# Kernel optimization log

Measured on AMD Instinct MI355X. Metric: run time of the kernel, lower is better.

## Reference

```python
import jax, jax.numpy as jnp
import numpy as np

N_NODES = 50000


def setup_inputs() -> dict:
    key = jax.random.key(0)
    ks = jax.random.split(key, 6)
    F_IN, F_HID, N_EDGES = 128, 512, 800000
    x = jax.random.normal(ks[0], (N_NODES, F_IN), dtype=jnp.float32)
    edge_index = jax.random.randint(ks[1], (2, N_EDGES), 0, N_NODES, dtype=jnp.int64)
    W1 = jax.random.normal(ks[2], (F_IN, F_HID), dtype=jnp.float32) * (1.0 / np.sqrt(F_IN))
    b1 = jnp.zeros((F_HID,), dtype=jnp.float32)
    W2 = jax.random.normal(ks[3], (F_HID, F_IN), dtype=jnp.float32) * (1.0 / np.sqrt(F_HID))
    b2 = jnp.zeros((F_IN,), dtype=jnp.float32)
    eps = jnp.zeros((), dtype=jnp.float32)  # train_eps=True, init 0
    return {"x": x, "edge_index": edge_index, "W1": W1, "b1": b1, "W2": W2, "b2": b2, "eps": eps}


def reference(x, edge_index, W1, b1, W2, b2, eps):
    # GINConv: out = MLP((1+eps)*x + sum_{j in N(i)} x_j)
    src, dst = edge_index[0], edge_index[1]
    agg = jax.ops.segment_sum(x[src], dst, num_segments=N_NODES)  # [N, F]
    h = (1.0 + eps) * x + agg
    h = jax.nn.relu(h @ W1 + b1)
    out = h @ W2 + b2
    return out
```

## Files before the change

kernel.cpp:

```cpp
#include <hip/hip_runtime.h>
#include <hip/hip_bf16.h>

#define N_NODES 50000
#define F_IN    128
#define F_HID   512
#define N_EDGES 800000

#define NBKT 782
#define RCAP 384
#define BINCAP 1280

typedef __bf16 bf16x2 __attribute__((ext_vector_type(2)));
typedef __bf16 bf16x4 __attribute__((ext_vector_type(4)));
typedef __bf16 bf16x8 __attribute__((ext_vector_type(8)));
typedef float  f32x4  __attribute__((ext_vector_type(4)));

#define NB_X 6250
#define NB_W 32
#define NB_CZ 98
__global__ __launch_bounds__(256) void prep(const float* __restrict__ x,
                                            const float* __restrict__ W1,
                                            const float* __restrict__ W2,
                                            __bf16* __restrict__ xb,
                                            __bf16* __restrict__ w1f,
                                            __bf16* __restrict__ w2f,
                                            int* __restrict__ bcnt) {
    int b = blockIdx.x, tid = threadIdx.x;
    if (b < NB_X) {
        int i = b * 256 + tid;
        float4 v = ((const float4*)x)[i];
        bf16x4 o = {(__bf16)v.x, (__bf16)v.y, (__bf16)v.z, (__bf16)v.w};
        ((bf16x4*)xb)[i] = o;
    } else if (b < NB_X + NB_W) {
        int t = (b - NB_X) * 256 + tid;
        int lane = t & 63, kk = (t >> 6) & 3, nt = (t >> 8) & 7, c = (t >> 11) & 3;
        int q = lane >> 4, l16 = lane & 15;
        bf16x8 o;
        #pragma unroll
        for (int j = 0; j < 8; ++j)
            o[j] = (__bf16)W1[(kk * 32 + q * 8 + j) * F_HID + c * 128 + nt * 16 + l16];
        *(bf16x8*)(w1f + (size_t)t * 8) = o;
    } else if (b < NB_X + 2 * NB_W) {
        int t = (b - NB_X - NB_W) * 256 + tid;
        int lane = t & 63, kk = (t >> 6) & 3, nt = (t >> 8) & 7, c = (t >> 11) & 3;
        int q = lane >> 4, l16 = lane & 15;
        bf16x8 o;
        #pragma unroll
        for (int j = 0; j < 8; ++j)
            o[j] = (__bf16)W2[(c * 128 + kk * 32 + q * 8 + j) * F_IN + nt * 16 + l16];
        *(bf16x8*)(w2f + (size_t)t * 8) = o;
    } else {
        int i = (b - NB_X - 2 * NB_W) * 256 + tid;
        if (i < NBKT * 8 * 4) {
            int4 z = {0, 0, 0, 0};
            ((int4*)bcnt)[i] = z;
        }
    }
}

__global__ __launch_bounds__(256) void bucket_fill(const int* __restrict__ ei,
                                                   int* __restrict__ bcnt,
                                                   int* __restrict__ entries) {
    int e = blockIdx.x * 256 + threadIdx.x;
    if (e >= N_EDGES) return;
    int src = ei[e];
    int dst = ei[N_EDGES + e];
    int cell = (dst >> 6) * 8 + (blockIdx.x & 7);
    int p = atomicAdd(&bcnt[cell * 16], 1);
    if (p < RCAP)
        entries[cell * RCAP + p] = ((dst & 63) << 16) | src;
}

__global__ __launch_bounds__(256) void bucket_bin(const int* __restrict__ bcnt,
                                                  const int* __restrict__ entries,
                                                  unsigned short* __restrict__ binned,
                                                  unsigned int* __restrict__ meta) {
    __shared__ int deg[64], base[64], cur[64];
    const int tid = threadIdx.x;
    const int bkt = blockIdx.x;

    if (tid < 64) deg[tid] = 0;
    __syncthreads();

    #pragma unroll
    for (int r = 0; r < 8; ++r) {
        int cnt = bcnt[(bkt * 8 + r) * 16];
        cnt = cnt < RCAP ? cnt : RCAP;
        const int* eb = entries + (size_t)(bkt * 8 + r) * RCAP;
        for (int i = tid; i < cnt; i += 256)
            atomicAdd(&deg[eb[i] >> 16], 1);
    }
    __syncthreads();

    if (tid == 0) {
        int s = 0;
        for (int n = 0; n < 64; ++n) { base[n] = s; s += deg[n]; }
    }
    __syncthreads();

    if (tid < 64) {
        cur[tid] = base[tid];
        int node = bkt * 64 + tid;
        if (node < N_NODES)
            meta[node] = ((unsigned int)deg[tid] << 20) | (unsigned int)(bkt * BINCAP + base[tid]);
    }
    __syncthreads();

    #pragma unroll
    for (int r = 0; r < 8; ++r) {
        int cnt = bcnt[(bkt * 8 + r) * 16];
        cnt = cnt < RCAP ? cnt : RCAP;
        const int* eb = entries + (size_t)(bkt * 8 + r) * RCAP;
        for (int i = tid; i < cnt; i += 256) {
            int en = eb[i];
            int p = atomicAdd(&cur[en >> 16], 1);
            if (p < BINCAP)
                binned[(size_t)bkt * BINCAP + p] = (unsigned short)(en & 0xffff);
        }
    }
}

__global__ __launch_bounds__(256) void gather_agg(const __bf16* __restrict__ xb,
                                                  const unsigned int* __restrict__ meta,
                                                  const unsigned short* __restrict__ binned,
                                                  const float* __restrict__ eps,
                                                  __bf16* __restrict__ agg) {
    int node = blockIdx.x * 4 + (threadIdx.x >> 6);
    int lane = threadIdx.x & 63;
    int q = lane >> 4, l16 = lane & 15;
    if (node >= N_NODES) return;
    const float s = 1.0f + eps[0];

    unsigned int m = meta[node];
    int deg = m >> 20;
    const unsigned short* bin = binned + (m & 0xFFFFF);

    float acc[8];
    #pragma unroll
    for (int i = 0; i < 8; ++i) acc[i] = 0.0f;
    if (q == 0) {
        bf16x8 self = *(const bf16x8*)(xb + (size_t)node * F_IN + l16 * 8);
        #pragma unroll
        for (int i = 0; i < 8; ++i) acc[i] = (float)self[i] * s;
    }

    int j = q;
    for (; j + 4 < deg; j += 8) {
        int s0 = bin[j];
        int s1 = bin[j + 4];
        bf16x8 v0 = *(const bf16x8*)(xb + (size_t)s0 * F_IN + l16 * 8);
        bf16x8 v1 = *(const bf16x8*)(xb + (size_t)s1 * F_IN + l16 * 8);
        #pragma unroll
        for (int i = 0; i < 8; ++i) acc[i] += (float)v0[i] + (float)v1[i];
    }
    if (j < deg) {
        bf16x8 v = *(const bf16x8*)(xb + (size_t)bin[j] * F_IN + l16 * 8);
        #pragma unroll
        for (int i = 0; i < 8; ++i) acc[i] += (float)v[i];
    }

    #pragma unroll
    for (int i = 0; i < 8; ++i) {
        acc[i] += __shfl_xor(acc[i], 16);
        acc[i] += __shfl_xor(acc[i], 32);
    }
    if (q == 0) {
        bf16x8 o;
        #pragma unroll
        for (int i = 0; i < 8; ++i) o[i] = (__bf16)acc[i];
        *(bf16x8*)(agg + (size_t)node * F_IN + l16 * 8) = o;
    }
}

__global__ __launch_bounds__(256) void fused_mlp(const __bf16* __restrict__ A,
                                                 const __bf16* __restrict__ w1f,
                                                 const __bf16* __restrict__ w2f,
                                                 const float* __restrict__ b1,
                                                 const float* __restrict__ b2,
                                                 float* __restrict__ out) {
    __shared__ __attribute__((aligned(16))) __bf16 Hb[4096];

    const int tid  = threadIdx.x;
    const int wave = tid >> 6;
    const int lane = tid & 63;
    const int q = lane >> 4, l16 = lane & 15;
    const int m0 = blockIdx.x * 32;

    bf16x8 a_reg[2][4];
    #pragma unroll
    for (int mi = 0; mi < 2; ++mi) {
        int m = m0 + mi * 16 + l16;
        #pragma unroll
        for (int kk = 0; kk < 4; ++kk) {
            if (m < N_NODES)
                a_reg[mi][kk] = *(const bf16x8*)(A + (size_t)m * F_IN + kk * 32 + q * 8);
            else {
                __bf16 z = (__bf16)0.0f;
                a_reg[mi][kk] = (bf16x8){z, z, z, z, z, z, z, z};
            }
        }
    }

    f32x4 acc_o[2][2];
    #pragma unroll
    for (int ni = 0; ni < 2; ++ni) {
        float bv = b2[wave * 32 + ni * 16 + l16];
        f32x4 b4 = {bv, bv, bv, bv};
        acc_o[0][ni] = b4;
        acc_o[1][ni] = b4;
    }

    for (int c = 0; c < 4; ++c) {
        f32x4 acc_h[2][2];
        #pragma unroll
        for (int ni = 0; ni < 2; ++ni) {
            float bv = b1[c * 128 + wave * 32 + ni * 16 + l16];
            f32x4 b4 = {bv, bv, bv, bv};
            acc_h[0][ni] = b4;
            acc_h[1][ni] = b4;
        }
        #pragma unroll
        for (int kk = 0; kk < 4; ++kk) {
            bf16x8 bw[2];
            #pragma unroll
            for (int ni = 0; ni < 2; ++ni)
                bw[ni] = *(const bf16x8*)(w1f +
                    ((size_t)((c * 8 + wave * 2 + ni) * 4 + kk) << 9) + lane * 8);
            #pragma unroll
            for (int mi = 0; mi < 2; ++mi)
                #pragma unroll
                for (int ni = 0; ni < 2; ++ni)
                    acc_h[mi][ni] = __builtin_amdgcn_mfma_f32_16x16x32_bf16(
                        a_reg[mi][kk], bw[ni], acc_h[mi][ni], 0, 0, 0);
        }
        #pragma unroll
        for (int mi = 0; mi < 2; ++mi)
            #pragma unroll
            for (int ni = 0; ni < 2; ++ni)
                #pragma unroll
                for (int r = 0; r < 4; ++r)
                    Hb[(((mi * 4 + wave) * 64 + (ni * 2 + (l16 >> 3)) * 16 + q * 4 + r) << 3)
                       + (l16 & 7)] = (__bf16)fmaxf(acc_h[mi][ni][r], 0.0f);
        __syncthreads();

        #pragma unroll
        for (int kk = 0; kk < 4; ++kk) {
            bf16x8 am[2], bw[2];
            #pragma unroll
            for (int mi = 0; mi < 2; ++mi)
                am[mi] = *(const bf16x8*)&Hb[((mi * 4 + kk) * 64 + lane) << 3];
            #pragma unroll
            for (int ni = 0; ni < 2; ++ni)
                bw[ni] = *(const bf16x8*)(w2f +
                    ((size_t)((c * 8 + wave * 2 + ni) * 4 + kk) << 9) + lane * 8);
            #pragma unroll
            for (int mi = 0; mi < 2; ++mi)
                #pragma unroll
                for (int ni = 0; ni < 2; ++ni)
                    acc_o[mi][ni] = __builtin_amdgcn_mfma_f32_16x16x32_bf16(
                        am[mi], bw[ni], acc_o[mi][ni], 0, 0, 0);
        }
        __syncthreads();
    }

    #pragma unroll
    for (int mi = 0; mi < 2; ++mi)
        #pragma unroll
        for (int ni = 0; ni < 2; ++ni)
            #pragma unroll
            for (int r = 0; r < 4; ++r) {
                int m = m0 + mi * 16 + q * 4 + r;
                if (m < N_NODES)
                    out[(size_t)m * F_IN + wave * 32 + ni * 16 + l16] = acc_o[mi][ni][r];
            }
}

extern "C" void kernel_launch(void* const* d_in, const int* in_sizes, int n_in,
                              void* d_out, int out_size, void* d_ws, size_t ws_size,
                              hipStream_t stream) {
    const float* x   = (const float*)d_in[0];
    const int*   ei  = (const int*)d_in[1];
    const float* W1  = (const float*)d_in[2];
    const float* b1  = (const float*)d_in[3];
    const float* W2  = (const float*)d_in[4];
    const float* b2  = (const float*)d_in[5];
    const float* eps = (const float*)d_in[6];
    float* out = (float*)d_out;

    char* ws = (char*)d_ws;
    __bf16* xb   = (__bf16*)ws;
    __bf16* agg  = (__bf16*)(ws + 12800000);
    __bf16* w1f  = (__bf16*)(ws + 25600000);
    __bf16* w2f  = (__bf16*)(ws + 25800000);
    int*    bcnt = (int*)(ws + 26000000);
    int*    entries = (int*)(ws + 26500000);
    unsigned int*   meta   = (unsigned int*)(ws + 36200000);
    unsigned short* binned = (unsigned short*)(ws + 36400000);

    prep<<<NB_X + 2 * NB_W + NB_CZ, 256, 0, stream>>>(x, W1, W2, xb, w1f, w2f, bcnt);
    bucket_fill<<<(N_EDGES + 255) / 256, 256, 0, stream>>>(ei, bcnt, entries);
    bucket_bin<<<NBKT, 256, 0, stream>>>(bcnt, entries, binned, meta);
    gather_agg<<<(N_NODES + 3) / 4, 256, 0, stream>>>(xb, meta, binned, eps, agg);
    fused_mlp<<<(N_NODES + 31) / 32, 256, 0, stream>>>(agg, w1f, w2f, b1, b2, out);
}
```

Before: 189.8 us.

## Fuse bucket binning, neighbor gather, and MLP into one per-bucket kernel

Merges bucket_bin, gather_agg and fused_mlp into a single 512-thread kernel, one block per 64-node bucket. The block bins the edges into shared memory, aggregates neighbor rows into a swizzled shared A tile, then runs both GEMMs from LDS. This removes the global round-trips for binned, meta and agg and two kernel launches. In exchange each block has only 782 blocks of 512 threads, uses more LDS, and serializes the gather and GEMM phases inside a block, which may lower overlap and occupancy.

```diff
diff --git a/kernel.cpp b/kernel.cpp
--- a/kernel.cpp
+++ b/kernel.cpp
@@ -71,140 +71,120 @@
         entries[cell * RCAP + p] = ((dst & 63) << 16) | src;
 }
 
-__global__ __launch_bounds__(256) void bucket_bin(const int* __restrict__ bcnt,
-                                                  const int* __restrict__ entries,
-                                                  unsigned short* __restrict__ binned,
-                                                  unsigned int* __restrict__ meta) {
-    __shared__ int deg[64], base[64], cur[64];
-    const int tid = threadIdx.x;
-    const int bkt = blockIdx.x;
-
-    if (tid < 64) deg[tid] = 0;
-    __syncthreads();
-
-    #pragma unroll
-    for (int r = 0; r < 8; ++r) {
-        int cnt = bcnt[(bkt * 8 + r) * 16];
-        cnt = cnt < RCAP ? cnt : RCAP;
-        const int* eb = entries + (size_t)(bkt * 8 + r) * RCAP;
-        for (int i = tid; i < cnt; i += 256)
-            atomicAdd(&deg[eb[i] >> 16], 1);
-    }
-    __syncthreads();
-
-    if (tid == 0) {
-        int s = 0;
-        for (int n = 0; n < 64; ++n) { base[n] = s; s += deg[n]; }
-    }
-    __syncthreads();
-
-    if (tid < 64) {
-        cur[tid] = base[tid];
-        int node = bkt * 64 + tid;
-        if (node < N_NODES)
-            meta[node] = ((unsigned int)deg[tid] << 20) | (unsigned int)(bkt * BINCAP + base[tid]);
-    }
-    __syncthreads();
-
-    #pragma unroll
-    for (int r = 0; r < 8; ++r) {
-        int cnt = bcnt[(bkt * 8 + r) * 16];
-        cnt = cnt < RCAP ? cnt : RCAP;
-        const int* eb = entries + (size_t)(bkt * 8 + r) * RCAP;
-        for (int i = tid; i < cnt; i += 256) {
-            int en = eb[i];
-            int p = atomicAdd(&cur[en >> 16], 1);
-            if (p < BINCAP)
-                binned[(size_t)bkt * BINCAP + p] = (unsigned short)(en & 0xffff);
-        }
-    }
-}
-
-__global__ __launch_bounds__(256) void gather_agg(const __bf16* __restrict__ xb,
-                                                  const unsigned int* __restrict__ meta,
-                                                  const unsigned short* __restrict__ binned,
-                                                  const float* __restrict__ eps,
-                                                  __bf16* __restrict__ agg) {
-    int node = blockIdx.x * 4 + (threadIdx.x >> 6);
-    int lane = threadIdx.x & 63;
-    int q = lane >> 4, l16 = lane & 15;
-    if (node >= N_NODES) return;
-    const float s = 1.0f + eps[0];
-
-    unsigned int m = meta[node];
-    int deg = m >> 20;
-    const unsigned short* bin = binned + (m & 0xFFFFF);
-
-    float acc[8];
-    #pragma unroll
-    for (int i = 0; i < 8; ++i) acc[i] = 0.0f;
-    if (q == 0) {
-        bf16x8 self = *(const bf16x8*)(xb + (size_t)node * F_IN + l16 * 8);
-        #pragma unroll
-        for (int i = 0; i < 8; ++i) acc[i] = (float)self[i] * s;
-    }
-
-    int j = q;
-    for (; j + 4 < deg; j += 8) {
-        int s0 = bin[j];
-        int s1 = bin[j + 4];
-        bf16x8 v0 = *(const bf16x8*)(xb + (size_t)s0 * F_IN + l16 * 8);
-        bf16x8 v1 = *(const bf16x8*)(xb + (size_t)s1 * F_IN + l16 * 8);
-        #pragma unroll
-        for (int i = 0; i < 8; ++i) acc[i] += (float)v0[i] + (float)v1[i];
-    }
-    if (j < deg) {
-        bf16x8 v = *(const bf16x8*)(xb + (size_t)bin[j] * F_IN + l16 * 8);
-        #pragma unroll
-        for (int i = 0; i < 8; ++i) acc[i] += (float)v[i];
-    }
-
-    #pragma unroll
-    for (int i = 0; i < 8; ++i) {
-        acc[i] += __shfl_xor(acc[i], 16);
-        acc[i] += __shfl_xor(acc[i], 32);
-    }
-    if (q == 0) {
-        bf16x8 o;
-        #pragma unroll
-        for (int i = 0; i < 8; ++i) o[i] = (__bf16)acc[i];
-        *(bf16x8*)(agg + (size_t)node * F_IN + l16 * 8) = o;
-    }
-}
-
-__global__ __launch_bounds__(256) void fused_mlp(const __bf16* __restrict__ A,
+__global__ __launch_bounds__(512) void gin_fused(const __bf16* __restrict__ xb,
+                                                 const int* __restrict__ bcnt,
+                                                 const int* __restrict__ entries,
+                                                 const float* __restrict__ eps,
                                                  const __bf16* __restrict__ w1f,
                                                  const __bf16* __restrict__ w2f,
                                                  const float* __restrict__ b1,
                                                  const float* __restrict__ b2,
                                                  float* __restrict__ out) {
-    __shared__ __attribute__((aligned(16))) __bf16 Hb[4096];
-
-    const int tid  = threadIdx.x;
-    const int wave = tid >> 6;
-    const int lane = tid & 63;
+    __shared__ int degs[64], bases[64], curs[64];
+    __shared__ unsigned short bin16[BINCAP];
+    __shared__ __attribute__((aligned(16))) __bf16 As[8192];
+    __shared__ __attribute__((aligned(16))) __bf16 Hb[8192];
+
+    const int tid = threadIdx.x;
+    const int wave = tid >> 6, lane = tid & 63;
     const int q = lane >> 4, l16 = lane & 15;
-    const int m0 = blockIdx.x * 32;
-
-    bf16x8 a_reg[2][4];
-    #pragma unroll
-    for (int mi = 0; mi < 2; ++mi) {
-        int m = m0 + mi * 16 + l16;
-        #pragma unroll
-        for (int kk = 0; kk < 4; ++kk) {
-            if (m < N_NODES)
-                a_reg[mi][kk] = *(const bf16x8*)(A + (size_t)m * F_IN + kk * 32 + q * 8);
-            else {
-                __bf16 z = (__bf16)0.0f;
-                a_reg[mi][kk] = (bf16x8){z, z, z, z, z, z, z, z};
-            }
-        }
-    }
+    const int bkt = blockIdx.x;
+
+    if (tid < 64) degs[tid] = 0;
+    __syncthreads();
+
+    int cnt = bcnt[(bkt * 8 + wave) * 16];
+    cnt = cnt < RCAP ? cnt : RCAP;
+    const int* eb = entries + (size_t)(bkt * 8 + wave) * RCAP;
+    int ev[6];
+    #pragma unroll
+    for (int u = 0; u < 6; ++u) {
+        int i = lane + u * 64;
+        int en = (i < cnt) ? eb[i] : -1;
+        ev[u] = en;
+        if (en >= 0) atomicAdd(&degs[en >> 16], 1);
+    }
+    __syncthreads();
+
+    if (wave == 0) {
+        int d = degs[lane];
+        int sum = d;
+        #pragma unroll
+        for (int off = 1; off < 64; off <<= 1) {
+            int t = __shfl_up(sum, off);
+            if (lane >= off) sum += t;
+        }
+        bases[lane] = sum - d;
+        curs[lane]  = sum - d;
+    }
+    __syncthreads();
+
+    #pragma unroll
+    for (int u = 0; u < 6; ++u) {
+        int en = ev[u];
+        if (en >= 0) {
+            int p = atomicAdd(&curs[en >> 16], 1);
+            if (p < BINCAP) bin16[p] = (unsigned short)(en & 0xffff);
+        }
+    }
+    __syncthreads();
+
+    const float s = 1.0f + eps[0];
+    for (int t = 0; t < 8; ++t) {
+        int n = wave * 8 + t;
+        int node = bkt * 64 + n;
+        if (node >= N_NODES) break;
+        int dg = degs[n], b0 = bases[n];
+        int end = b0 + dg;
+        end = end < BINCAP ? end : BINCAP;
+
+        float acc[8];
+        #pragma unroll
+        for (int i = 0; i < 8; ++i) acc[i] = 0.0f;
+        if (q == 0) {
+            bf16x8 self = *(const bf16x8*)(xb + (size_t)node * F_IN + l16 * 8);
+            #pragma unroll
+            for (int i = 0; i < 8; ++i) acc[i] = (float)self[i] * s;
+        }
+
+        int j = b0 + q;
+        for (; j + 4 < end; j += 8) {
+            int s0 = bin16[j];
+            int s1 = bin16[j + 4];
+            bf16x8 r0 = *(const bf16x8*)(xb + (size_t)s0 * F_IN + l16 * 8);
+            bf16x8 r1 = *(const bf16x8*)(xb + (size_t)s1 * F_IN + l16 * 8);
+            #pragma unroll
+            for (int i = 0; i < 8; ++i) acc[i] += (float)r0[i] + (float)r1[i];
+        }
+        if (j < end) {
+            bf16x8 r0 = *(const bf16x8*)(xb + (size_t)bin16[j] * F_IN + l16 * 8);
+            #pragma unroll
+            for (int i = 0; i < 8; ++i) acc[i] += (float)r0[i];
+        }
+
+        #pragma unroll
+        for (int i = 0; i < 8; ++i) {
+            acc[i] += __shfl_xor(acc[i], 16);
+            acc[i] += __shfl_xor(acc[i], 32);
+        }
+        if (lane < 16) {
+            int g = n >> 4, r16 = n & 15;
+            bf16x8 o;
+            #pragma unroll
+            for (int i = 0; i < 8; ++i) o[i] = (__bf16)acc[i];
+            int byte = (g * 16 + lane) * 256 + r16 * 16;
+            byte ^= (lane & 7) << 4;
+            *(bf16x8*)((char*)As + byte) = o;
+        }
+    }
+    __syncthreads();
+
+    const int wr = wave >> 2, wc = wave & 3;
 
     f32x4 acc_o[2][2];
     #pragma unroll
     for (int ni = 0; ni < 2; ++ni) {
-        float bv = b2[wave * 32 + ni * 16 + l16];
+        float bv = b2[wc * 32 + ni * 16 + l16];
         f32x4 b4 = {bv, bv, bv, bv};
         acc_o[0][ni] = b4;
         acc_o[1][ni] = b4;
@@ -214,33 +194,42 @@
         f32x4 acc_h[2][2];
         #pragma unroll
         for (int ni = 0; ni < 2; ++ni) {
-            float bv = b1[c * 128 + wave * 32 + ni * 16 + l16];
+            float bv = b1[c * 128 + wc * 32 + ni * 16 + l16];
             f32x4 b4 = {bv, bv, bv, bv};
             acc_h[0][ni] = b4;
             acc_h[1][ni] = b4;
         }
         #pragma unroll
         for (int kk = 0; kk < 4; ++kk) {
-            bf16x8 bw[2];
+            bf16x8 am[2], bw[2];
+            #pragma unroll
+            for (int mi = 0; mi < 2; ++mi) {
+                int g = wr * 2 + mi;
+                int byte = ((g * 4 + kk) * 4 + q) * 256 + l16 * 16;
+                byte ^= ((kk * 4 + q) & 7) << 4;
+                am[mi] = *(const bf16x8*)((const char*)As + byte);
+            }
             #pragma unroll
             for (int ni = 0; ni < 2; ++ni)
                 bw[ni] = *(const bf16x8*)(w1f +
-                    ((size_t)((c * 8 + wave * 2 + ni) * 4 + kk) << 9) + lane * 8);
+                    ((size_t)((c * 8 + wc * 2 + ni) * 4 + kk) << 9) + lane * 8);
             #pragma unroll
             for (int mi = 0; mi < 2; ++mi)
                 #pragma unroll
                 for (int ni = 0; ni < 2; ++ni)
                     acc_h[mi][ni] = __builtin_amdgcn_mfma_f32_16x16x32_bf16(
-                        a_reg[mi][kk], bw[ni], acc_h[mi][ni], 0, 0, 0);
-        }
-        #pragma unroll
-        for (int mi = 0; mi < 2; ++mi)
+                        am[mi], bw[ni], acc_h[mi][ni], 0, 0, 0);
+        }
+        #pragma unroll
+        for (int mi = 0; mi < 2; ++mi) {
+            int g = wr * 2 + mi;
             #pragma unroll
             for (int ni = 0; ni < 2; ++ni)
                 #pragma unroll
                 for (int r = 0; r < 4; ++r)
-                    Hb[(((mi * 4 + wave) * 64 + (ni * 2 + (l16 >> 3)) * 16 + q * 4 + r) << 3)
+                    Hb[(((g * 4 + wc) * 64 + (ni * 2 + (l16 >> 3)) * 16 + q * 4 + r) << 3)
                        + (l16 & 7)] = (__bf16)fmaxf(acc_h[mi][ni][r], 0.0f);
+        }
         __syncthreads();
 
         #pragma unroll
@@ -248,11 +237,11 @@
             bf16x8 am[2], bw[2];
             #pragma unroll
             for (int mi = 0; mi < 2; ++mi)
-                am[mi] = *(const bf16x8*)&Hb[((mi * 4 + kk) * 64 + lane) << 3];
+                am[mi] = *(const bf16x8*)&Hb[(((wr * 2 + mi) * 4 + kk) * 64 + lane) << 3];
             #pragma unroll
             for (int ni = 0; ni < 2; ++ni)
                 bw[ni] = *(const bf16x8*)(w2f +
-                    ((size_t)((c * 8 + wave * 2 + ni) * 4 + kk) << 9) + lane * 8);
+                    ((size_t)((c * 8 + wc * 2 + ni) * 4 + kk) << 9) + lane * 8);
             #pragma unroll
             for (int mi = 0; mi < 2; ++mi)
                 #pragma unroll
@@ -263,15 +252,16 @@
         __syncthreads();
     }
 
+    const int m0 = bkt * 64;
     #pragma unroll
     for (int mi = 0; mi < 2; ++mi)
         #pragma unroll
         for (int ni = 0; ni < 2; ++ni)
             #pragma unroll
             for (int r = 0; r < 4; ++r) {
-                int m = m0 + mi * 16 + q * 4 + r;
+                int m = m0 + wr * 32 + mi * 16 + q * 4 + r;
                 if (m < N_NODES)
-                    out[(size_t)m * F_IN + wave * 32 + ni * 16 + l16] = acc_o[mi][ni][r];
+                    out[(size_t)m * F_IN + wc * 32 + ni * 16 + l16] = acc_o[mi][ni][r];
             }
 }
 
@@ -289,17 +279,12 @@
 
     char* ws = (char*)d_ws;
     __bf16* xb   = (__bf16*)ws;
-    __bf16* agg  = (__bf16*)(ws + 12800000);
-    __bf16* w1f  = (__bf16*)(ws + 25600000);
-    __bf16* w2f  = (__bf16*)(ws + 25800000);
-    int*    bcnt = (int*)(ws + 26000000);
-    int*    entries = (int*)(ws + 26500000);
-    unsigned int*   meta   = (unsigned int*)(ws + 36200000);
-    unsigned short* binned = (unsigned short*)(ws + 36400000);
+    __bf16* w1f  = (__bf16*)(ws + 12800000);
+    __bf16* w2f  = (__bf16*)(ws + 13000000);
+    int*    bcnt = (int*)(ws + 13200000);
+    int*    entries = (int*)(ws + 13700000);
 
     prep<<<NB_X + 2 * NB_W + NB_CZ, 256, 0, stream>>>(x, W1, W2, xb, w1f, w2f, bcnt);
     bucket_fill<<<(N_EDGES + 255) / 256, 256, 0, stream>>>(ei, bcnt, entries);
-    bucket_bin<<<NBKT, 256, 0, stream>>>(bcnt, entries, binned, meta);
-    gather_agg<<<(N_NODES + 3) / 4, 256, 0, stream>>>(xb, meta, binned, eps, agg);
-    fused_mlp<<<(N_NODES + 31) / 32, 256, 0, stream>>>(agg, w1f, w2f, b1, b2, out);
-}
+    gin_fused<<<NBKT, 512, 0, stream>>>(xb, bcnt, entries, eps, w1f, w2f, b1, b2, out);
+}
```

New measurement: 187.4 us. Within noise of the previous version (-1.2%).
